# Optimization experiments

Measured on AMD Instinct MI355X. Metric: run time of the kernel, lower is better.

Reference implementation:

```python
import jax, jax.numpy as jnp
import numpy as np

N_NODES = 100000
N_EDGES = 1600000
D_IN = 64
D_HID = 64


def setup_inputs() -> dict:
    key = jax.random.key(0)
    k1, k2, k3, k4, k5 = jax.random.split(key, 5)
    features = jax.random.normal(k1, (N_NODES, D_IN), dtype=jnp.float32)
    src = jax.random.randint(k2, (N_EDGES,), 0, N_NODES, dtype=jnp.int64)
    dst = jax.random.randint(k3, (N_EDGES,), 0, N_NODES, dtype=jnp.int64)
    # nn.Linear(in_feats, n_hidden): W is [out, in], b is [out]
    W = jax.random.normal(k4, (D_HID, D_IN), dtype=jnp.float32) * (1.0 / np.sqrt(D_IN))
    b = jax.random.normal(k5, (D_HID,), dtype=jnp.float32) * 0.01
    return {"features": features, "src": src, "dst": dst, "W": W, "b": b}


def reference(features, src, dst, W, b):
    # copy_src + sum: h_agg[v] = sum_{(u->v) in E} features[u]
    msgs = features[src]                                   # [E, D_IN] gather
    h_agg = jax.ops.segment_sum(msgs, dst, num_segments=N_NODES)  # [N, D_IN] scatter-add
    # NodeApplyModule: linear + activation
    h = h_agg @ W.T + b                                    # [N, D_HID]
    return jax.nn.relu(h)
```

## Files before the change

kernel.cpp:

```cpp
#include <hip/hip_runtime.h>
#include <hip/hip_bf16.h>

constexpr int N_NODES = 100000;
constexpr int N_EDGES = 1600000;
constexpr int D = 64;
constexpr int NPB = 64;
constexpr int NBUK = (N_NODES + NPB - 1) / NPB;
constexpr int CAP = 1536;
constexpr int PART_BLOCKS = 256;
constexpr int PART_THREADS = 1024;
constexpr int EPB = (N_EDGES + PART_BLOCKS - 1) / PART_BLOCKS;

__device__ inline unsigned pack_bf16_2(float a, float b) {
    unsigned ua = __float_as_uint(a), ub = __float_as_uint(b);
    ua = (ua + 0x7FFFu + ((ua >> 16) & 1u)) >> 16;
    ub = (ub + 0x7FFFu + ((ub >> 16) & 1u)) >> 16;
    return ua | (ub << 16);
}

__global__ __launch_bounds__(256) void convert_kernel(
    const float* __restrict__ feat, uint2* __restrict__ fb) {
    const int total = N_NODES * D / 4;
    const float4* f4 = reinterpret_cast<const float4*>(feat);
    for (int i = blockIdx.x * 256 + threadIdx.x; i < total; i += gridDim.x * 256) {
        const float4 v = f4[i];
        fb[i] = make_uint2(pack_bf16_2(v.x, v.y), pack_bf16_2(v.z, v.w));
    }
}

__global__ __launch_bounds__(PART_THREADS) void partition_kernel(
    const int* __restrict__ src, const int* __restrict__ dst,
    int* __restrict__ gtot, unsigned* __restrict__ packed) {
    __shared__ int lcnt[NBUK];
    __shared__ int lbase[NBUK];

    const int tid = threadIdx.x;
    const int lo = blockIdx.x * EPB;
    int hi = lo + EPB; if (hi > N_EDGES) hi = N_EDGES;

    for (int i = tid; i < NBUK; i += PART_THREADS) lcnt[i] = 0;
    __syncthreads();

    #pragma unroll 4
    for (int e = lo + tid; e < hi; e += PART_THREADS)
        atomicAdd(&lcnt[dst[e] >> 6], 1);
    __syncthreads();

    for (int i = tid; i < NBUK; i += PART_THREADS) {
        const int c = lcnt[i];
        lbase[i] = c ? atomicAdd(&gtot[i], c) : 0;
        lcnt[i] = 0;
    }
    __syncthreads();

    #pragma unroll 4
    for (int e = lo + tid; e < hi; e += PART_THREADS) {
        const int d = dst[e];
        const int buk = d >> 6;
        const int p = lbase[buk] + atomicAdd(&lcnt[buk], 1);
        if (p < CAP)
            packed[(size_t)buk * CAP + p] =
                ((unsigned)(d & (NPB - 1)) << 17) | (unsigned)src[e];
    }
}

__global__ __launch_bounds__(256, 2) void bucket_kernel(
    const uint2* __restrict__ fb, const int* __restrict__ gtot,
    const unsigned* __restrict__ packed, const float* __restrict__ W,
    const float* __restrict__ bias, float* __restrict__ out) {
    __shared__ unsigned elist[CAP];
    __shared__ int cnt[NPB];
    __shared__ int cur[NPB];
    __shared__ int inc[NPB];
    __shared__ float hrow[4][D];

    const int tid = threadIdx.x;
    const int w = tid >> 6;
    const int j = tid & 63;
    const int g = j >> 4;
    const int l = j & 15;
    const int buk = blockIdx.x;

    float4 wr[16];
    #pragma unroll
    for (int q = 0; q < 16; ++q)
        wr[q] = *reinterpret_cast<const float4*>(W + j * D + (q << 2));
    const float bj = bias[j];

    int m = gtot[buk]; if (m > CAP) m = CAP;
    const unsigned* bp = packed + (size_t)buk * CAP;

    if (tid < NPB) cnt[tid] = 0;
    __syncthreads();

    #pragma unroll 4
    for (int i = tid; i < m; i += 256)
        atomicAdd(&cnt[bp[i] >> 17], 1);
    __syncthreads();

    if (tid < 64) {
        const int c = cnt[tid];
        int x = c;
        #pragma unroll
        for (int o = 1; o < 64; o <<= 1) {
            const int y = __shfl_up(x, o);
            if (tid >= o) x += y;
        }
        inc[tid] = x;
        cur[tid] = x - c;
    }
    __syncthreads();

    #pragma unroll 4
    for (int i = tid; i < m; i += 256) {
        const unsigned pk = bp[i];
        const int p = atomicAdd(&cur[pk >> 17], 1);
        elist[p] = pk & 0x1FFFFu;
    }
    __syncthreads();

    const int gbase = buk * NPB;

    for (int n = w; n < NPB; n += 4) {
        const int gn = gbase + n;
        if (gn >= N_NODES) break;
        const int e1 = inc[n];
        int i = e1 - cnt[n];

        float hx = 0.f, hy = 0.f, hz = 0.f, hw_ = 0.f;

        for (; i + 16 <= e1; i += 16) {
            const int s0 = elist[i + g];
            const int s1 = elist[i + 4 + g];
            const int s2 = elist[i + 8 + g];
            const int s3 = elist[i + 12 + g];
            const uint2 q0 = fb[(size_t)s0 * 16 + l];
            const uint2 q1 = fb[(size_t)s1 * 16 + l];
            const uint2 q2 = fb[(size_t)s2 * 16 + l];
            const uint2 q3 = fb[(size_t)s3 * 16 + l];
            hx += __uint_as_float(q0.x << 16) + __uint_as_float(q1.x << 16)
                + __uint_as_float(q2.x << 16) + __uint_as_float(q3.x << 16);
            hy += __uint_as_float(q0.x & 0xFFFF0000u) + __uint_as_float(q1.x & 0xFFFF0000u)
                + __uint_as_float(q2.x & 0xFFFF0000u) + __uint_as_float(q3.x & 0xFFFF0000u);
            hz += __uint_as_float(q0.y << 16) + __uint_as_float(q1.y << 16)
                + __uint_as_float(q2.y << 16) + __uint_as_float(q3.y << 16);
            hw_ += __uint_as_float(q0.y & 0xFFFF0000u) + __uint_as_float(q1.y & 0xFFFF0000u)
                 + __uint_as_float(q2.y & 0xFFFF0000u) + __uint_as_float(q3.y & 0xFFFF0000u);
        }
        if (i + 8 <= e1) {
            const int s0 = elist[i + g];
            const int s1 = elist[i + 4 + g];
            const uint2 q0 = fb[(size_t)s0 * 16 + l];
            const uint2 q1 = fb[(size_t)s1 * 16 + l];
            hx += __uint_as_float(q0.x << 16) + __uint_as_float(q1.x << 16);
            hy += __uint_as_float(q0.x & 0xFFFF0000u) + __uint_as_float(q1.x & 0xFFFF0000u);
            hz += __uint_as_float(q0.y << 16) + __uint_as_float(q1.y << 16);
            hw_ += __uint_as_float(q0.y & 0xFFFF0000u) + __uint_as_float(q1.y & 0xFFFF0000u);
            i += 8;
        }
        if (i + 4 <= e1) {
            const uint2 q0 = fb[(size_t)elist[i + g] * 16 + l];
            hx += __uint_as_float(q0.x << 16);
            hy += __uint_as_float(q0.x & 0xFFFF0000u);
            hz += __uint_as_float(q0.y << 16);
            hw_ += __uint_as_float(q0.y & 0xFFFF0000u);
            i += 4;
        }
        const int rem = e1 - i;
        if (g < rem) {
            const uint2 q0 = fb[(size_t)elist[i + g] * 16 + l];
            hx += __uint_as_float(q0.x << 16);
            hy += __uint_as_float(q0.x & 0xFFFF0000u);
            hz += __uint_as_float(q0.y << 16);
            hw_ += __uint_as_float(q0.y & 0xFFFF0000u);
        }

        hx += __shfl_xor(hx, 16); hx += __shfl_xor(hx, 32);
        hy += __shfl_xor(hy, 16); hy += __shfl_xor(hy, 32);
        hz += __shfl_xor(hz, 16); hz += __shfl_xor(hz, 32);
        hw_ += __shfl_xor(hw_, 16); hw_ += __shfl_xor(hw_, 32);

        if (g == 0)
            *reinterpret_cast<float4*>(&hrow[w][l << 2]) =
                make_float4(hx, hy, hz, hw_);

        float acc = bj;
        #pragma unroll
        for (int q = 0; q < 16; ++q) {
            const float4 hv = *reinterpret_cast<const float4*>(&hrow[w][q << 2]);
            acc = fmaf(hv.x, wr[q].x, acc);
            acc = fmaf(hv.y, wr[q].y, acc);
            acc = fmaf(hv.z, wr[q].z, acc);
            acc = fmaf(hv.w, wr[q].w, acc);
        }
        out[(size_t)gn * D + j] = fmaxf(acc, 0.0f);
    }
}

extern "C" void kernel_launch(void* const* d_in, const int* in_sizes, int n_in,
                              void* d_out, int out_size, void* d_ws, size_t ws_size,
                              hipStream_t stream) {
    const float* feat = (const float*)d_in[0];
    const int*   src  = (const int*)d_in[1];
    const int*   dst  = (const int*)d_in[2];
    const float* W    = (const float*)d_in[3];
    const float* b    = (const float*)d_in[4];
    float* out = (float*)d_out;

    int* gtot = (int*)d_ws;
    unsigned* packed = (unsigned*)((char*)d_ws + 8192);
    uint2* fb = (uint2*)((char*)d_ws + 8192 + (size_t)NBUK * CAP * 4);

    hipMemsetAsync(gtot, 0, NBUK * sizeof(int), stream);

    convert_kernel<<<2048, 256, 0, stream>>>(feat, fb);

    partition_kernel<<<PART_BLOCKS, PART_THREADS, 0, stream>>>(src, dst, gtot, packed);

    bucket_kernel<<<NBUK, 256, 0, stream>>>(fb, gtot, packed, W, b, out);
}
```

Measured before the change: 110.3 us.

## Fuse convert and partition kernels; pad per-node edge lists with zero sentinel

Merges the bf16 feature conversion and the edge partition into one launch, with the extra blocks doing conversion, so the two run concurrently and one launch is saved. In the bucket kernel each node's edge list is padded to a multiple of 16 with a sentinel index that points at an all-zero feature row. This lets the gather loop drop its tail branches. The cost is extra padded gathers of the zero row, a larger shared edge list, and initialising that list to the sentinel.

```diff
diff --git a/kernel.cpp b/kernel.cpp
--- a/kernel.cpp
+++ b/kernel.cpp
@@ -7,8 +7,11 @@
 constexpr int NPB = 64;
 constexpr int NBUK = (N_NODES + NPB - 1) / NPB;
 constexpr int CAP = 1536;
+constexpr int CAP_E = 2304;
+constexpr unsigned SENT = 100000u;
 constexpr int PART_BLOCKS = 256;
-constexpr int PART_THREADS = 1024;
+constexpr int CONV_BLOCKS = 64;
+constexpr int PREP_THREADS = 1024;
 constexpr int EPB = (N_EDGES + PART_BLOCKS - 1) / PART_BLOCKS;
 
 __device__ inline unsigned pack_bf16_2(float a, float b) {
@@ -18,35 +21,40 @@
     return ua | (ub << 16);
 }
 
-__global__ __launch_bounds__(256) void convert_kernel(
-    const float* __restrict__ feat, uint2* __restrict__ fb) {
-    const int total = N_NODES * D / 4;
-    const float4* f4 = reinterpret_cast<const float4*>(feat);
-    for (int i = blockIdx.x * 256 + threadIdx.x; i < total; i += gridDim.x * 256) {
-        const float4 v = f4[i];
-        fb[i] = make_uint2(pack_bf16_2(v.x, v.y), pack_bf16_2(v.z, v.w));
-    }
-}
-
-__global__ __launch_bounds__(PART_THREADS) void partition_kernel(
-    const int* __restrict__ src, const int* __restrict__ dst,
-    int* __restrict__ gtot, unsigned* __restrict__ packed) {
+__global__ __launch_bounds__(PREP_THREADS) void prep_kernel(
+    const float* __restrict__ feat, const int* __restrict__ src,
+    const int* __restrict__ dst, int* __restrict__ gtot,
+    unsigned* __restrict__ packed, uint2* __restrict__ fb) {
+    const int tid = threadIdx.x;
+
+    if (blockIdx.x >= PART_BLOCKS) {
+        const int cb = blockIdx.x - PART_BLOCKS;
+        const int total = N_NODES * D / 4;
+        const float4* f4 = reinterpret_cast<const float4*>(feat);
+        for (int i = cb * PREP_THREADS + tid; i < total; i += CONV_BLOCKS * PREP_THREADS) {
+            const float4 v = f4[i];
+            fb[i] = make_uint2(pack_bf16_2(v.x, v.y), pack_bf16_2(v.z, v.w));
+        }
+        if (cb == 0 && tid < 16)
+            fb[(size_t)SENT * 16 + tid] = make_uint2(0u, 0u);
+        return;
+    }
+
     __shared__ int lcnt[NBUK];
     __shared__ int lbase[NBUK];
 
-    const int tid = threadIdx.x;
     const int lo = blockIdx.x * EPB;
     int hi = lo + EPB; if (hi > N_EDGES) hi = N_EDGES;
 
-    for (int i = tid; i < NBUK; i += PART_THREADS) lcnt[i] = 0;
-    __syncthreads();
-
-    #pragma unroll 4
-    for (int e = lo + tid; e < hi; e += PART_THREADS)
+    for (int i = tid; i < NBUK; i += PREP_THREADS) lcnt[i] = 0;
+    __syncthreads();
+
+    #pragma unroll 4
+    for (int e = lo + tid; e < hi; e += PREP_THREADS)
         atomicAdd(&lcnt[dst[e] >> 6], 1);
     __syncthreads();
 
-    for (int i = tid; i < NBUK; i += PART_THREADS) {
+    for (int i = tid; i < NBUK; i += PREP_THREADS) {
         const int c = lcnt[i];
         lbase[i] = c ? atomicAdd(&gtot[i], c) : 0;
         lcnt[i] = 0;
@@ -54,7 +62,7 @@
     __syncthreads();
 
     #pragma unroll 4
-    for (int e = lo + tid; e < hi; e += PART_THREADS) {
+    for (int e = lo + tid; e < hi; e += PREP_THREADS) {
         const int d = dst[e];
         const int buk = d >> 6;
         const int p = lbase[buk] + atomicAdd(&lcnt[buk], 1);
@@ -68,10 +76,10 @@
     const uint2* __restrict__ fb, const int* __restrict__ gtot,
     const unsigned* __restrict__ packed, const float* __restrict__ W,
     const float* __restrict__ bias, float* __restrict__ out) {
-    __shared__ unsigned elist[CAP];
+    __shared__ unsigned elist[CAP_E];
     __shared__ int cnt[NPB];
     __shared__ int cur[NPB];
-    __shared__ int inc[NPB];
+    __shared__ int pstart[NPB];
     __shared__ float hrow[4][D];
 
     const int tid = threadIdx.x;
@@ -91,6 +99,7 @@
     const unsigned* bp = packed + (size_t)buk * CAP;
 
     if (tid < NPB) cnt[tid] = 0;
+    for (int i = tid; i < CAP_E; i += 256) elist[i] = SENT;
     __syncthreads();
 
     #pragma unroll 4
@@ -100,14 +109,15 @@
 
     if (tid < 64) {
         const int c = cnt[tid];
-        int x = c;
+        const int pc = (c + 15) & ~15;
+        int x = pc;
         #pragma unroll
         for (int o = 1; o < 64; o <<= 1) {
             const int y = __shfl_up(x, o);
             if (tid >= o) x += y;
         }
-        inc[tid] = x;
-        cur[tid] = x - c;
+        pstart[tid] = x - pc;
+        cur[tid] = x - pc;
     }
     __syncthreads();
 
@@ -124,12 +134,12 @@
     for (int n = w; n < NPB; n += 4) {
         const int gn = gbase + n;
         if (gn >= N_NODES) break;
-        const int e1 = inc[n];
-        int i = e1 - cnt[n];
+        const int i0 = pstart[n];
+        const int e1 = i0 + ((cnt[n] + 15) & ~15);
 
         float hx = 0.f, hy = 0.f, hz = 0.f, hw_ = 0.f;
 
-        for (; i + 16 <= e1; i += 16) {
+        for (int i = i0; i < e1; i += 16) {
             const int s0 = elist[i + g];
             const int s1 = elist[i + 4 + g];
             const int s2 = elist[i + 8 + g];
@@ -147,33 +157,6 @@
             hw_ += __uint_as_float(q0.y & 0xFFFF0000u) + __uint_as_float(q1.y & 0xFFFF0000u)
                  + __uint_as_float(q2.y & 0xFFFF0000u) + __uint_as_float(q3.y & 0xFFFF0000u);
         }
-        if (i + 8 <= e1) {
-            const int s0 = elist[i + g];
-            const int s1 = elist[i + 4 + g];
-            const uint2 q0 = fb[(size_t)s0 * 16 + l];
-            const uint2 q1 = fb[(size_t)s1 * 16 + l];
-            hx += __uint_as_float(q0.x << 16) + __uint_as_float(q1.x << 16);
-            hy += __uint_as_float(q0.x & 0xFFFF0000u) + __uint_as_float(q1.x & 0xFFFF0000u);
-            hz += __uint_as_float(q0.y << 16) + __uint_as_float(q1.y << 16);
-            hw_ += __uint_as_float(q0.y & 0xFFFF0000u) + __uint_as_float(q1.y & 0xFFFF0000u);
-            i += 8;
-        }
-        if (i + 4 <= e1) {
-            const uint2 q0 = fb[(size_t)elist[i + g] * 16 + l];
-            hx += __uint_as_float(q0.x << 16);
-            hy += __uint_as_float(q0.x & 0xFFFF0000u);
-            hz += __uint_as_float(q0.y << 16);
-            hw_ += __uint_as_float(q0.y & 0xFFFF0000u);
-            i += 4;
-        }
-        const int rem = e1 - i;
-        if (g < rem) {
-            const uint2 q0 = fb[(size_t)elist[i + g] * 16 + l];
-            hx += __uint_as_float(q0.x << 16);
-            hy += __uint_as_float(q0.x & 0xFFFF0000u);
-            hz += __uint_as_float(q0.y << 16);
-            hw_ += __uint_as_float(q0.y & 0xFFFF0000u);
-        }
 
         hx += __shfl_xor(hx, 16); hx += __shfl_xor(hx, 32);
         hy += __shfl_xor(hy, 16); hy += __shfl_xor(hy, 32);
@@ -213,9 +196,8 @@
 
     hipMemsetAsync(gtot, 0, NBUK * sizeof(int), stream);
 
-    convert_kernel<<<2048, 256, 0, stream>>>(feat, fb);
-
-    partition_kernel<<<PART_BLOCKS, PART_THREADS, 0, stream>>>(src, dst, gtot, packed);
+    prep_kernel<<<PART_BLOCKS + CONV_BLOCKS, PREP_THREADS, 0, stream>>>(
+        feat, src, dst, gtot, packed, fb);
 
     bucket_kernel<<<NBUK, 256, 0, stream>>>(fb, gtot, packed, W, b, out);
 }
```

New measurement: 101.7 us. -7.7%, faster.
